# Kernel tuning notes

Hardware: AMD Instinct MI355X
Metric: run time of the kernel (lower is better)

Reference implementation:

```python
import jax, jax.numpy as jnp
import numpy as np

D_MODEL = 1024

def setup_inputs() -> dict:
    key = jax.random.key(0)
    kx, kq, kk, kv, ko = jax.random.split(key, 5)
    x = jax.random.normal(kx, (4, 4096, D_MODEL), dtype=jnp.float32)
    w_q = jax.random.normal(kq, (D_MODEL, D_MODEL), dtype=jnp.float32)
    w_k = jax.random.normal(kk, (D_MODEL, D_MODEL), dtype=jnp.float32)
    w_v = jax.random.normal(kv, (D_MODEL, D_MODEL), dtype=jnp.float32)
    w_o = jax.random.normal(ko, (D_MODEL, D_MODEL), dtype=jnp.float32)
    return {"x": x, "w_q": w_q, "w_k": w_k, "w_v": w_v, "w_o": w_o}

def reference(x, w_q, w_k, w_v, w_o):
    # Q/K/V projections: [B,T,D] @ [D,D] -> [B,T,D]
    q = jnp.einsum('btd,de->bte', x, w_q)
    k = jnp.einsum('btd,de->bte', x, w_k)
    v = jnp.einsum('btd,de->bte', x, w_v)
    # Unnormalized attention: scores [B,T,T] (no softmax)
    scores = jnp.einsum('btd,bsd->bts', q, k)
    attn_output = jnp.einsum('bts,bsd->btd', scores, v)
    # Output projection
    output = jnp.einsum('btd,de->bte', attn_output, w_o)
    return output
```

## Files before the change

### kernel.cpp

```cpp
#include <hip/hip_runtime.h>
#include <hip/hip_bf16.h>
#include <stdint.h>

typedef unsigned short u16;
typedef short bf16x8 __attribute__((ext_vector_type(8)));
typedef float f32x4 __attribute__((ext_vector_type(4)));

#define GLOAD16(gp, lp) __builtin_amdgcn_global_load_lds( \
    (const __attribute__((address_space(1))) uint32_t*)(gp), \
    (__attribute__((address_space(3))) uint32_t*)(lp), 16, 0, 0)

#define VMCNT10 do { asm volatile("s_waitcnt vmcnt(10)" ::: "memory"); \
                     __builtin_amdgcn_sched_barrier(0); } while (0)
#define SBAR    do { __builtin_amdgcn_s_barrier(); \
                     __builtin_amdgcn_sched_barrier(0); } while (0)
#define LGKM0   do { asm volatile("s_waitcnt lgkmcnt(0)" ::: "memory"); \
                     __builtin_amdgcn_sched_barrier(0); } while (0)

__device__ __forceinline__ u16 f2bf(float f) {
  union { float f; uint32_t u; } x; x.f = f;
  return (u16)((x.u + 0x7FFFu + ((x.u >> 16) & 1u)) >> 16);
}
__device__ __forceinline__ float bf2f(u16 h) {
  union { uint32_t u; float f; } x; x.u = (uint32_t)h << 16;
  return x.f;
}

__device__ __forceinline__ void xcd_swizzle(int& bx, int& by, int& bz) {
  const int gx = gridDim.x, gy = gridDim.y;
  const int nwg = gx * gy * (int)gridDim.z;
  const int lin = ((int)blockIdx.z * gy + (int)blockIdx.y) * gx + (int)blockIdx.x;
  const int q = nwg >> 3;
  const int wl = (lin & 7) * q + (lin >> 3);
  bz = wl / (gx * gy);
  const int rem = wl - bz * gx * gy;
  by = rem / gx;
  bx = rem - by * gx;
}

__global__ __launch_bounds__(512) void cast_x_all(const float* __restrict__ x,
                                                  const float* __restrict__ wq,
                                                  const float* __restrict__ wk,
                                                  const float* __restrict__ wv,
                                                  const float* __restrict__ wo,
                                                  u16* __restrict__ xb,
                                                  u16* __restrict__ xTt,
                                                  u16* __restrict__ WA,
                                                  u16* __restrict__ WBb) {
  __shared__ u16 ldsT[73728];
  const int b = blockIdx.x;
  const int t = threadIdx.x;
  const int t0 = b * 64;

  const int fA = (t & 7) << 3;
  const int d2 = t * 2;
  const int rowA0 = d2 * 72;
  const int rowA1 = rowA0 + 72;
  for (int j = 0; j < 64; ++j) {
    float2 v = *(const float2*)&x[(size_t)(t0 + j) * 1024 + d2];
    u16 p0 = f2bf(v.x), p1 = f2bf(v.y);
    *(uint32_t*)&xb[(size_t)(t0 + j) * 1024 + d2] =
        (uint32_t)p0 | ((uint32_t)p1 << 16);
    const int jc = j ^ fA;
    ldsT[rowA0 + jc] = p0;
    ldsT[rowA1 + jc] = p1;
  }
  __syncthreads();

#pragma unroll
  for (int k = 0; k < 16; ++k) {
    const int idx = k * 4096 + t * 8;
    const int tile = idx >> 13;
    const int o = idx & 8191;
    const int dl = o >> 6, c = o & 63;
    const int d = tile * 128 + dl;
    const int f = ((dl >> 1) & 7) << 3;
    uint4 val = *(const uint4*)&ldsT[d * 72 + (c ^ f)];
    *(uint4*)&xTt[((size_t)(tile * 256 + b)) * 8192 + dl * 64 + c] = val;
  }

#pragma unroll
  for (int r = 0; r < 3; ++r) {
    const int e = b * 12288 + r * 4096 + t * 8;
    const int w = e >> 20, loc = e & 1048575;
    const float* in = w == 0 ? wq : w == 1 ? wk : wv;
    u16* o2 = w == 0 ? WA : w == 1 ? WBb : WBb + 1048576;
    float4 a = *(const float4*)&in[loc];
    float4 c4 = *(const float4*)&in[loc + 4];
    u16 p[8];
    p[0] = f2bf(a.x);  p[1] = f2bf(a.y);  p[2] = f2bf(a.z);  p[3] = f2bf(a.w);
    p[4] = f2bf(c4.x); p[5] = f2bf(c4.y); p[6] = f2bf(c4.z); p[7] = f2bf(c4.w);
    *(uint4*)&o2[loc] = *(const uint4*)p;
  }

  __syncthreads();
  float (*tf)[65] = (float(*)[65])ldsT;
  const int r0 = (b >> 4) * 64, c0 = (b & 15) * 64;
  const int lr = t >> 3, lc = (t & 7) * 8;
  {
    const float* src = wo + (size_t)(r0 + lr) * 1024 + c0 + lc;
    float4 v0 = *(const float4*)&src[0];
    float4 v1 = *(const float4*)&src[4];
    tf[lr][lc + 0] = v0.x; tf[lr][lc + 1] = v0.y;
    tf[lr][lc + 2] = v0.z; tf[lr][lc + 3] = v0.w;
    tf[lr][lc + 4] = v1.x; tf[lr][lc + 5] = v1.y;
    tf[lr][lc + 6] = v1.z; tf[lr][lc + 7] = v1.w;
  }
  __syncthreads();
  {
    u16 tr[8];
#pragma unroll
    for (int j = 0; j < 8; ++j) tr[j] = f2bf(tf[lc + j][lr]);
    u16* dst = WA + 1048576 + (size_t)(c0 + lr) * 1024 + r0 + lc;
    *(uint4*)&dst[0] = *(const uint4*)tr;
  }
}

__global__ __launch_bounds__(512) void gram_w12(const u16* __restrict__ xTt,
                                                u16* __restrict__ Gp,
                                                const u16* __restrict__ WA,
                                                const u16* __restrict__ WBb,
                                                u16* __restrict__ W12) {
  __shared__ u16 lds[2 * 8192];
  const int lin = blockIdx.x;
  const int wl = (lin & 7) * 88 + (lin >> 3);
  const u16 *Abase, *Bbase;
  u16* Cb;
  int lda, sKt, ldc;
  if (wl < 576) {
    const int z = wl / 36, t5 = wl - z * 36;
    const int b = z >> 2, kc = z & 3;
    int ti = 0;
    while ((ti + 1) * (ti + 2) / 2 <= t5) ++ti;
    const int tj = t5 - ti * (ti + 1) / 2;
    const int tc0 = b * 64 + kc * 16;
    Abase = xTt + (size_t)(ti * 256 + tc0) * 8192;
    Bbase = xTt + (size_t)(tj * 256 + tc0) * 8192;
    lda = 64; sKt = 8192;
    Cb = Gp + ((size_t)z * 36 + t5) * 16384;
    ldc = 128;
  } else {
    const int w = wl - 576;
    const int z2 = w >> 6, tl = w & 63;
    const int by = tl >> 3, bx = tl & 7;
    Abase = WA + (size_t)z2 * 1048576 + (size_t)(by * 128) * 1024;
    Bbase = WBb + (size_t)z2 * 1048576 + (size_t)(bx * 128) * 1024;
    lda = 1024; sKt = 64;
    Cb = W12 + (size_t)z2 * 1048576 + (size_t)(by * 128) * 1024 + bx * 128;
    ldc = 1024;
  }

  const int t = threadIdx.x;
  const int l = t & 63;
  const int wid = t >> 6;
  const int wr = wid >> 2, wc = wid & 3;
  const int lr16 = l & 15, hi = l >> 4;

  f32x4 acc[4][2];
#pragma unroll
  for (int m = 0; m < 4; ++m)
#pragma unroll
    for (int n = 0; n < 2; ++n) acc[m][n] = (f32x4){0.f, 0.f, 0.f, 0.f};

  for (int s = 0; s < 16; ++s) {
    __syncthreads();
    const u16* As = Abase + (size_t)s * sKt;
    const u16* Bs = Bbase + (size_t)s * sKt;
#pragma unroll
    for (int i = 0; i < 2; ++i) {
      int slot = i * 512 + t;
      int row = slot >> 3, cp = slot & 7;
      int clog = cp ^ (row & 7);
      GLOAD16(As + (size_t)row * lda + clog * 8, &lds[slot * 8]);
    }
#pragma unroll
    for (int i = 0; i < 2; ++i) {
      int slot = i * 512 + t;
      int row = slot >> 3, cp = slot & 7;
      int clog = cp ^ (row & 7);
      GLOAD16(Bs + (size_t)row * lda + clog * 8, &lds[8192 + slot * 8]);
    }
    asm volatile("s_waitcnt vmcnt(0)" ::: "memory");
    __syncthreads();
#pragma unroll
    for (int ks = 0; ks < 2; ++ks) {
      bf16x8 af[4], bfr[2];
#pragma unroll
      for (int m = 0; m < 4; ++m) {
        int row = wr * 64 + m * 16 + lr16;
        int p = (ks * 4 + hi) ^ (row & 7);
        af[m] = *(const bf16x8*)&lds[row * 64 + p * 8];
      }
#pragma unroll
      for (int n = 0; n < 2; ++n) {
        int row = wc * 32 + n * 16 + lr16;
        int p = (ks * 4 + hi) ^ (row & 7);
        bfr[n] = *(const bf16x8*)&lds[8192 + row * 64 + p * 8];
      }
#pragma unroll
      for (int m = 0; m < 4; ++m)
#pragma unroll
        for (int n = 0; n < 2; ++n)
          acc[m][n] = __builtin_amdgcn_mfma_f32_16x16x32_bf16(af[m], bfr[n], acc[m][n], 0, 0, 0);
    }
  }

#pragma unroll
  for (int m = 0; m < 4; ++m) {
    int row0 = wr * 64 + m * 16 + hi * 4;
#pragma unroll
    for (int n = 0; n < 2; ++n) {
      int col = wc * 32 + n * 16 + lr16;
      f32x4 v = acc[m][n];
#pragma unroll
      for (int r = 0; r < 4; ++r) Cb[(size_t)(row0 + r) * ldc + col] = f2bf(v[r]);
    }
  }
}

__global__ __launch_bounds__(512) void gemm_bt8(const u16* __restrict__ A,
                                                const u16* __restrict__ B,
                                                u16* __restrict__ C,
                                                int lda, int ldb, int ldc, int K,
                                                size_t sA, size_t sB, size_t sC) {
  __shared__ u16 lds[2 * 8192];
  int bx, by, bz;
  xcd_swizzle(bx, by, bz);
  A += (size_t)bz * sA;
  B += (size_t)bz * sB;
  const int t = threadIdx.x;
  const int l = t & 63;
  const int wid = t >> 6;
  const int wr = wid >> 2, wc = wid & 3;
  const int lr16 = l & 15, hi = l >> 4;
  const int mBase = by * 128;
  const int nBase = bx * 128;

  f32x4 acc[4][2];
#pragma unroll
  for (int m = 0; m < 4; ++m)
#pragma unroll
    for (int n = 0; n < 2; ++n) acc[m][n] = (f32x4){0.f, 0.f, 0.f, 0.f};

  for (int kt = 0; kt < K; kt += 64) {
    __syncthreads();
#pragma unroll
    for (int i = 0; i < 2; ++i) {
      int s = i * 512 + t;
      int row = s >> 3, cp = s & 7;
      int clog = cp ^ (row & 7);
      GLOAD16(A + (size_t)(mBase + row) * lda + kt + clog * 8, &lds[s * 8]);
    }
#pragma unroll
    for (int i = 0; i < 2; ++i) {
      int s = i * 512 + t;
      int row = s >> 3, cp = s & 7;
      int clog = cp ^ (row & 7);
      GLOAD16(B + (size_t)(nBase + row) * ldb + kt + clog * 8, &lds[8192 + s * 8]);
    }
    asm volatile("s_waitcnt vmcnt(0)" ::: "memory");
    __syncthreads();
#pragma unroll
    for (int ks = 0; ks < 2; ++ks) {
      bf16x8 af[4], bfr[2];
#pragma unroll
      for (int m = 0; m < 4; ++m) {
        int row = wr * 64 + m * 16 + lr16;
        int p = (ks * 4 + hi) ^ (row & 7);
        af[m] = *(const bf16x8*)&lds[row * 64 + p * 8];
      }
#pragma unroll
      for (int n = 0; n < 2; ++n) {
        int row = wc * 32 + n * 16 + lr16;
        int p = (ks * 4 + hi) ^ (row & 7);
        bfr[n] = *(const bf16x8*)&lds[8192 + row * 64 + p * 8];
      }
#pragma unroll
      for (int m = 0; m < 4; ++m)
#pragma unroll
        for (int n = 0; n < 2; ++n)
          acc[m][n] = __builtin_amdgcn_mfma_f32_16x16x32_bf16(af[m], bfr[n], acc[m][n], 0, 0, 0);
    }
  }

#pragma unroll
  for (int m = 0; m < 4; ++m) {
    int row0 = mBase + wr * 64 + m * 16 + hi * 4;
#pragma unroll
    for (int n = 0; n < 2; ++n) {
      int col = nBase + wc * 32 + n * 16 + lr16;
      f32x4 v = acc[m][n];
      u16* Cb = C + (size_t)bz * sC;
#pragma unroll
      for (int r = 0; r < 4; ++r) Cb[(size_t)(row0 + r) * ldc + col] = f2bf(v[r]);
    }
  }
}

__global__ __launch_bounds__(256) void reduce_mirror(const u16* __restrict__ Gp,
                                                     u16* __restrict__ G) {
  __shared__ u16 ldsT[128][136];
  const int t5 = blockIdx.x;
  const int b = blockIdx.y;
  int ti = 0;
  while ((ti + 1) * (ti + 2) / 2 <= t5) ++ti;
  const int tj = t5 - ti * (ti + 1) / 2;
  const int tid = threadIdx.x;
  const int rr = tid >> 4, ccc = (tid & 15) * 8;
  u16* Gb = G + (size_t)b * 1048576;
  const size_t ZS = (size_t)36 * 16384;
  const u16* base = Gp + ((size_t)(b * 4) * 36 + t5) * 16384;
#pragma unroll
  for (int i = 0; i < 8; ++i) {
    int row = i * 16 + rr;
    const u16* p = base + row * 128 + ccc;
    u16 a0[8], a1[8], a2[8], a3[8], o[8];
    *(uint4*)a0 = *(const uint4*)&p[0];
    *(uint4*)a1 = *(const uint4*)&p[ZS];
    *(uint4*)a2 = *(const uint4*)&p[2 * ZS];
    *(uint4*)a3 = *(const uint4*)&p[3 * ZS];
#pragma unroll
    for (int j = 0; j < 8; ++j)
      o[j] = f2bf(bf2f(a0[j]) + bf2f(a1[j]) + bf2f(a2[j]) + bf2f(a3[j]));
    *(uint4*)&Gb[(size_t)(ti * 128 + row) * 1024 + tj * 128 + ccc] = *(const uint4*)o;
    *(uint4*)&ldsT[row][ccc] = *(const uint4*)o;
  }
  if (ti != tj) {
    __syncthreads();
#pragma unroll
    for (int i = 0; i < 8; ++i) {
      int row = i * 16 + rr;
      u16 m8[8];
#pragma unroll
      for (int j = 0; j < 8; ++j) m8[j] = ldsT[ccc + j][row];
      *(uint4*)&Gb[(size_t)(tj * 128 + row) * 1024 + ti * 128 + ccc] = *(const uint4*)m8;
    }
  }
}

template <bool F32OUT>
__device__ __forceinline__ void gemm256_core(const u16* __restrict__ A,
                                             const u16* __restrict__ B,
                                             void* __restrict__ C,
                                             int lda, int ldb, int ldc, int K,
                                             int mBase, int nBase, u16* lds) {
  const int t = threadIdx.x;
  const int l = t & 63;
  const int wid = t >> 6;
  const int wr = wid >> 2;
  const int wc = wid & 3;
  const int lr16 = l & 15, hi = l >> 4;
  const int rl0 = t >> 3;
  const int rl1 = rl0 + 64;
  const int cp  = t & 7;
  const int cs  = cp ^ (rl0 & 7);
  const int NT = K >> 6;

  f32x4 acc[8][4];
#pragma unroll
  for (int m = 0; m < 8; ++m)
#pragma unroll
    for (int n = 0; n < 4; ++n) acc[m][n] = (f32x4){0.f, 0.f, 0.f, 0.f};

  auto stage = [&](const u16* g0, int ld, u16* d) {
    GLOAD16(g0 + (size_t)rl0 * ld + cs * 8, d + rl0 * 64 + cp * 8);
    GLOAD16(g0 + (size_t)rl1 * ld + cs * 8, d + rl1 * 64 + cp * 8);
  };
  stage(A + (size_t)mBase * lda,          lda, lds + 0);
  stage(B + (size_t)nBase * ldb,          ldb, lds + 16384);
  stage(B + (size_t)(nBase + 128) * ldb,  ldb, lds + 24576);
  stage(A + (size_t)(mBase + 128) * lda,  lda, lds + 8192);
  stage(B + (size_t)nBase * ldb + 64,         ldb, lds + 32768 + 16384);
  stage(A + (size_t)mBase * lda + 64,         lda, lds + 32768);
  stage(B + (size_t)(nBase + 128) * ldb + 64, ldb, lds + 32768 + 24576);

  bf16x8 af[4][2], b0[2][2], b1[2][2];

  for (int tt = 0; tt < NT; ++tt) {
    const int cur = tt & 1;
    u16* bufA = lds + cur * 32768;
    u16* bufB = bufA + 16384;
    u16* bufN = lds + ((tt + 1) & 1) * 32768;
    int t1 = tt + 1; if (t1 >= NT) t1 -= NT;
    int t2 = tt + 2; if (t2 >= NT) t2 -= NT;
    const int k1 = t1 * 64, k2 = t2 * 64;

    VMCNT10;
    SBAR;
    stage(A + (size_t)(mBase + 128) * lda + k1, lda, bufN + 8192);
#pragma unroll
    for (int mi = 0; mi < 4; ++mi) {
      int row = wr * 64 + mi * 16 + lr16;
#pragma unroll
      for (int kk = 0; kk < 2; ++kk) {
        int p = (kk * 4 + hi) ^ (row & 7);
        af[mi][kk] = *(const bf16x8*)&bufA[row * 64 + p * 8];
      }
    }
#pragma unroll
    for (int ni = 0; ni < 2; ++ni) {
      int row = wc * 32 + ni * 16 + lr16;
#pragma unroll
      for (int kk = 0; kk < 2; ++kk) {
        int p = (kk * 4 + hi) ^ (row & 7);
        b0[ni][kk] = *(const bf16x8*)&bufB[row * 64 + p * 8];
      }
    }
    LGKM0;
    __builtin_amdgcn_s_setprio(1);
#pragma unroll
    for (int kk = 0; kk < 2; ++kk)
#pragma unroll
      for (int mi = 0; mi < 4; ++mi)
#pragma unroll
        for (int ni = 0; ni < 2; ++ni)
          acc[mi][ni] = __builtin_amdgcn_mfma_f32_16x16x32_bf16(af[mi][kk], b0[ni][kk], acc[mi][ni], 0, 0, 0);
    __builtin_amdgcn_s_setprio(0);

    VMCNT10;
    SBAR;
    stage(B + (size_t)nBase * ldb + k2, ldb, bufB);
#pragma unroll
    for (int ni = 0; ni < 2; ++ni) {
      int row = 128 + wc * 32 + ni * 16 + lr16;
#pragma unroll
      for (int kk = 0; kk < 2; ++kk) {
        int p = (kk * 4 + hi) ^ (row & 7);
        b1[ni][kk] = *(const bf16x8*)&bufB[row * 64 + p * 8];
      }
    }
    LGKM0;
    __builtin_amdgcn_s_setprio(1);
#pragma unroll
    for (int kk = 0; kk < 2; ++kk)
#pragma unroll
      for (int mi = 0; mi < 4; ++mi)
#pragma unroll
        for (int ni = 0; ni < 2; ++ni)
          acc[mi][2 + ni] = __builtin_amdgcn_mfma_f32_16x16x32_bf16(af[mi][kk], b1[ni][kk], acc[mi][2 + ni], 0, 0, 0);
    __builtin_amdgcn_s_setprio(0);

    VMCNT10;
    SBAR;
    stage(A + (size_t)mBase * lda + k2, lda, bufA);
#pragma unroll
    for (int mi = 0; mi < 4; ++mi) {
      int row = 128 + wr * 64 + mi * 16 + lr16;
#pragma unroll
      for (int kk = 0; kk < 2; ++kk) {
        int p = (kk * 4 + hi) ^ (row & 7);
        af[mi][kk] = *(const bf16x8*)&bufA[row * 64 + p * 8];
      }
    }
    LGKM0;
    __builtin_amdgcn_s_setprio(1);
#pragma unroll
    for (int kk = 0; kk < 2; ++kk)
#pragma unroll
      for (int mi = 0; mi < 4; ++mi)
#pragma unroll
        for (int ni = 0; ni < 2; ++ni)
          acc[4 + mi][2 + ni] = __builtin_amdgcn_mfma_f32_16x16x32_bf16(af[mi][kk], b1[ni][kk], acc[4 + mi][2 + ni], 0, 0, 0);
    __builtin_amdgcn_s_setprio(0);

    SBAR;
    stage(B + (size_t)(nBase + 128) * ldb + k2, ldb, bufB + 8192);
    __builtin_amdgcn_s_setprio(1);
#pragma unroll
    for (int kk = 0; kk < 2; ++kk)
#pragma unroll
      for (int mi = 0; mi < 4; ++mi)
#pragma unroll
        for (int ni = 0; ni < 2; ++ni)
          acc[4 + mi][ni] = __builtin_amdgcn_mfma_f32_16x16x32_bf16(af[mi][kk], b0[ni][kk], acc[4 + mi][ni], 0, 0, 0);
    __builtin_amdgcn_s_setprio(0);
  }

#pragma unroll
  for (int m = 0; m < 8; ++m) {
    int row0 = mBase + (m >> 2) * 128 + wr * 64 + (m & 3) * 16 + hi * 4;
#pragma unroll
    for (int n = 0; n < 4; ++n) {
      int col = nBase + (n >> 1) * 128 + wc * 32 + (n & 1) * 16 + lr16;
      f32x4 v = acc[m][n];
      if (F32OUT) {
        float* Cf = (float*)C;
#pragma unroll
        for (int r = 0; r < 4; ++r) Cf[(size_t)(row0 + r) * ldc + col] = v[r];
      } else {
        u16* Cb = (u16*)C;
#pragma unroll
        for (int r = 0; r < 4; ++r) Cb[(size_t)(row0 + r) * ldc + col] = f2bf(v[r]);
      }
    }
  }
}

__global__ __launch_bounds__(512) void gemm256_out(const u16* __restrict__ xb,
                                                   const u16* __restrict__ PT,
                                                   float* __restrict__ out) {
  __shared__ u16 lds[65536];
  int bx, by, bz;
  xcd_swizzle(bx, by, bz);
  const u16* Bp = PT + (size_t)(by >> 4) * 1048576;
  gemm256_core<true>(xb, Bp, out, 1024, 1024, 1024, 1024, by * 256, bx * 256, lds);
}

extern "C" void kernel_launch(void* const* d_in, const int* in_sizes, int n_in,
                              void* d_out, int out_size, void* d_ws, size_t ws_size,
                              hipStream_t stream) {
  const float* x  = (const float*)d_in[0];
  const float* wq = (const float*)d_in[1];
  const float* wk = (const float*)d_in[2];
  const float* wv = (const float*)d_in[3];
  const float* wo = (const float*)d_in[4];
  float* out = (float*)d_out;

  u16* ws = (u16*)d_ws;
  const size_t MW = 1048576;
  u16* xb  = ws;
  u16* xTt = ws + 16 * MW;
  u16* WA  = ws + 32 * MW;
  u16* WBb = ws + 34 * MW;
  u16* W12 = ws + 36 * MW;
  u16* G   = ws + 38 * MW;
  u16* S   = ws + 42 * MW;
  u16* PT  = ws + 46 * MW;
  u16* Gp  = ws + 50 * MW;

  cast_x_all<<<256, 512, 0, stream>>>(x, wq, wk, wv, wo, xb, xTt, WA, WBb);

  gram_w12<<<704, 512, 0, stream>>>(xTt, Gp, WA, WBb, W12);
  reduce_mirror<<<dim3(36, 4), 256, 0, stream>>>(Gp, G);

  gemm_bt8<<<dim3(8, 8, 4), 512, 0, stream>>>(W12 + MW, G, S,
                                              1024, 1024, 1024, 1024,
                                              0, MW, MW);
  gemm_bt8<<<dim3(8, 8, 4), 512, 0, stream>>>(S, W12, PT,
                                              1024, 1024, 1024, 1024,
                                              MW, 0, MW);
  gemm256_out<<<dim3(4, 64), 512, 0, stream>>>(xb, PT, out);
}
```

Before: 148.2 us.

## Double-buffer LDS tiles in gemm_bt8 to overlap global loads with MFMA

Converts the bt8 GEMM main loop from single-buffered load-wait-compute into a double-buffered pipeline. The next K tile is prefetched into the alternate LDS buffer while MFMAs run on the current one, which removes one barrier per iteration. It also raises wave priority around the MFMA block with s_setprio. LDS use doubles to 64KB per block, which may lower occupancy.

New measurement: 138.7 us. -6.4%, faster.

```diff
diff --git a/kernel.cpp b/kernel.cpp
--- a/kernel.cpp
+++ b/kernel.cpp
@@ -223,18 +223,32 @@
                                                 u16* __restrict__ C,
                                                 int lda, int ldb, int ldc, int K,
                                                 size_t sA, size_t sB, size_t sC) {
-  __shared__ u16 lds[2 * 8192];
+  __shared__ u16 lds[4 * 8192];
   int bx, by, bz;
   xcd_swizzle(bx, by, bz);
-  A += (size_t)bz * sA;
-  B += (size_t)bz * sB;
+  const u16* Ab = A + (size_t)bz * sA + (size_t)(by * 128) * lda;
+  const u16* Bb = B + (size_t)bz * sB + (size_t)(bx * 128) * ldb;
   const int t = threadIdx.x;
   const int l = t & 63;
   const int wid = t >> 6;
   const int wr = wid >> 2, wc = wid & 3;
   const int lr16 = l & 15, hi = l >> 4;
-  const int mBase = by * 128;
-  const int nBase = bx * 128;
+
+  const int r0s = t >> 3, cp = t & 7;
+  const int cs = cp ^ (r0s & 7);
+
+  auto stage = [&](const u16* gA, const u16* gB, int kt, u16* d) {
+#pragma unroll
+    for (int i = 0; i < 2; ++i) {
+      int row = i * 64 + r0s;
+      GLOAD16(gA + (size_t)row * lda + kt + cs * 8, d + (i * 512 + t) * 8);
+    }
+#pragma unroll
+    for (int i = 0; i < 2; ++i) {
+      int row = i * 64 + r0s;
+      GLOAD16(gB + (size_t)row * ldb + kt + cs * 8, d + 8192 + (i * 512 + t) * 8);
+    }
+  };
 
   f32x4 acc[4][2];
 #pragma unroll
@@ -242,24 +256,14 @@
 #pragma unroll
     for (int n = 0; n < 2; ++n) acc[m][n] = (f32x4){0.f, 0.f, 0.f, 0.f};
 
+  stage(Ab, Bb, 0, lds);
+  asm volatile("s_waitcnt vmcnt(0)" ::: "memory");
+  __syncthreads();
+
+  int cur = 0;
   for (int kt = 0; kt < K; kt += 64) {
-    __syncthreads();
-#pragma unroll
-    for (int i = 0; i < 2; ++i) {
-      int s = i * 512 + t;
-      int row = s >> 3, cp = s & 7;
-      int clog = cp ^ (row & 7);
-      GLOAD16(A + (size_t)(mBase + row) * lda + kt + clog * 8, &lds[s * 8]);
-    }
-#pragma unroll
-    for (int i = 0; i < 2; ++i) {
-      int s = i * 512 + t;
-      int row = s >> 3, cp = s & 7;
-      int clog = cp ^ (row & 7);
-      GLOAD16(B + (size_t)(nBase + row) * ldb + kt + clog * 8, &lds[8192 + s * 8]);
-    }
-    asm volatile("s_waitcnt vmcnt(0)" ::: "memory");
-    __syncthreads();
+    if (kt + 64 < K) stage(Ab, Bb, kt + 64, lds + (cur ^ 1) * 16384);
+    const u16* cb = lds + cur * 16384;
 #pragma unroll
     for (int ks = 0; ks < 2; ++ks) {
       bf16x8 af[4], bfr[2];
@@ -267,28 +271,33 @@
       for (int m = 0; m < 4; ++m) {
         int row = wr * 64 + m * 16 + lr16;
         int p = (ks * 4 + hi) ^ (row & 7);
-        af[m] = *(const bf16x8*)&lds[row * 64 + p * 8];
+        af[m] = *(const bf16x8*)&cb[row * 64 + p * 8];
       }
 #pragma unroll
       for (int n = 0; n < 2; ++n) {
         int row = wc * 32 + n * 16 + lr16;
         int p = (ks * 4 + hi) ^ (row & 7);
-        bfr[n] = *(const bf16x8*)&lds[8192 + row * 64 + p * 8];
-      }
+        bfr[n] = *(const bf16x8*)&cb[8192 + row * 64 + p * 8];
+      }
+      __builtin_amdgcn_s_setprio(1);
 #pragma unroll
       for (int m = 0; m < 4; ++m)
 #pragma unroll
         for (int n = 0; n < 2; ++n)
           acc[m][n] = __builtin_amdgcn_mfma_f32_16x16x32_bf16(af[m], bfr[n], acc[m][n], 0, 0, 0);
-    }
+      __builtin_amdgcn_s_setprio(0);
+    }
+    asm volatile("s_waitcnt vmcnt(0)" ::: "memory");
+    __syncthreads();
+    cur ^= 1;
   }
 
 #pragma unroll
   for (int m = 0; m < 4; ++m) {
-    int row0 = mBase + wr * 64 + m * 16 + hi * 4;
+    int row0 = by * 128 + wr * 64 + m * 16 + hi * 4;
 #pragma unroll
     for (int n = 0; n < 2; ++n) {
-      int col = nBase + wc * 32 + n * 16 + lr16;
+      int col = bx * 128 + wc * 32 + n * 16 + lr16;
       f32x4 v = acc[m][n];
       u16* Cb = C + (size_t)bz * sC;
 #pragma unroll
```
